# Optimization experiments

Hardware: AMD Instinct MI355X
Metric: run time of the kernel (lower is better)

## Reference

```python
import jax, jax.numpy as jnp
import numpy as np

B, C, H, W = 32, 256, 64, 64
AS = 8  # attn_size


def _avgpool(x, s):
    # exact adaptive avg pool when H,W divisible by s: mean over each block
    b, c, h, w = x.shape
    return x.reshape(b, c, s, h // s, s, w // s).mean(axis=(3, 5))


def setup_inputs() -> dict:
    key = jax.random.key(0)
    ks = jax.random.split(key, 6)
    scale = 1.0 / np.sqrt(C)
    return {
        "F_rgb": jax.random.normal(ks[0], (B, C, H, W), jnp.float32),
        "F_d": jax.random.normal(ks[1], (B, C, H, W), jnp.float32),
        "Wq": jax.random.normal(ks[2], (C, C), jnp.float32) * scale,
        "bq": jnp.zeros((C,), jnp.float32),
        "Wk": jax.random.normal(ks[3], (C, C), jnp.float32) * scale,
        "bk": jnp.zeros((C,), jnp.float32),
        "Wv": jax.random.normal(ks[4], (C, C), jnp.float32) * scale,
        "bv": jnp.zeros((C,), jnp.float32),
        "alpha": jnp.float32(0.5),
    }


def reference(F_rgb, F_d, Wq, bq, Wk, bk, Wv, bv, alpha):
    b, c, h_in, w_in = F_rgb.shape
    R = _avgpool(F_rgb, AS)  # [B,C,8,8]
    D = _avgpool(F_d, AS)    # [B,C,8,8]
    # 1x1 convs == channel-mixing matmuls
    Q = jnp.einsum('oc,bchw->bohw', Wq, R) + bq[None, :, None, None]
    K = jnp.einsum('oc,bchw->bohw', Wk, D) + bk[None, :, None, None]
    V = jnp.einsum('oc,bchw->bohw', Wv, D) + bv[None, :, None, None]
    T = AS * AS
    Qf = Q.reshape(b, c, T)
    Kf = K.reshape(b, c, T)
    Vf = V.reshape(b, c, T)
    A = jnp.einsum('bct,bcs->bts', Qf, Kf)        # [B,T,T]
    A = jax.nn.softmax(A, axis=-1)
    Fatt = jnp.einsum('bcs,bts->bct', Vf, A)      # V @ A^T
    Fatt = Fatt.reshape(b, c, AS, AS)
    # bilinear upsample, half-pixel centers (== torch align_corners=False)
    Fatt = jax.image.resize(Fatt, (b, c, h_in, w_in), method='bilinear')
    return alpha * Fatt + (1.0 - alpha) * F_rgb
```

## Files before the change

### kernel.cpp

```cpp
#include <hip/hip_runtime.h>
#include <math.h>

#define B_  32
#define C_  256
#define T_  64
#define HW_ 4096

__global__ __launch_bounds__(256) void k_pool(const float* __restrict__ Frgb,
                                              const float* __restrict__ Fd,
                                              float* __restrict__ R,
                                              float* __restrict__ D) {
    __shared__ float P[2][1024];
    const int tid = threadIdx.x;
    const int plane = blockIdx.x;
    const float4* pr = (const float4*)Frgb + (size_t)plane * 1024;
    const float4* pd = (const float4*)Fd   + (size_t)plane * 1024;
    #pragma unroll
    for (int k = 0; k < 4; ++k) {
        float4 a = pr[k*256 + tid];
        P[0][k*256 + tid] = a.x + a.y + a.z + a.w;
        float4 b = pd[k*256 + tid];
        P[1][k*256 + tid] = b.x + b.y + b.z + b.w;
    }
    __syncthreads();
    if (tid < 128) {
        const int tensor = tid >> 6;
        const int cell = tid & 63;
        const int cy = cell >> 3, cx = cell & 7;
        const int base = (cy >> 1)*256 + (cy & 1)*128 + 2*cx;
        float s = 0.f;
        #pragma unroll
        for (int rg = 0; rg < 8; ++rg)
            s += P[tensor][base + rg*16] + P[tensor][base + rg*16 + 1];
        float* dst = tensor ? D : R;
        dst[(size_t)plane*64 + cell] = s * (1.f/64.f);
    }
}

__global__ __launch_bounds__(256) void k_qkv(const float* __restrict__ R, const float* __restrict__ D,
                                             const float* __restrict__ Wq, const float* __restrict__ bq,
                                             const float* __restrict__ Wk, const float* __restrict__ bk,
                                             const float* __restrict__ Wv, const float* __restrict__ bv,
                                             float* __restrict__ Q, float* __restrict__ K,
                                             float* __restrict__ V) {
    __shared__ float Ws[32 * 256];
    const int tid = threadIdx.x;
    const int tbase = blockIdx.x * 16;
    const int b = blockIdx.y;
    const int z = blockIdx.z;
    const float* W    = (z == 0) ? Wq : (z == 1) ? Wk : Wv;
    const float* bias = (z == 0) ? bq : (z == 1) ? bk : bv;
    const float* X    = (z == 0) ? R  : D;
    float* Out        = (z == 0) ? Q  : (z == 1) ? K  : V;

    const int o = tid;
    float acc[16];
    const float bz = bias[o];
    #pragma unroll
    for (int t = 0; t < 16; ++t) acc[t] = bz;

    const float* Xb = X + (size_t)b * C_ * T_;
    for (int cb = 0; cb < 256; cb += 32) {
        __syncthreads();
        #pragma unroll
        for (int k = 0; k < 8; ++k) {
            float4 w4 = *(const float4*)(W + (size_t)o * 256 + cb + k*4);
            Ws[(k*4 + 0)*256 + o] = w4.x;
            Ws[(k*4 + 1)*256 + o] = w4.y;
            Ws[(k*4 + 2)*256 + o] = w4.z;
            Ws[(k*4 + 3)*256 + o] = w4.w;
        }
        __syncthreads();
        for (int cl = 0; cl < 32; ++cl) {
            const float w = Ws[cl*256 + o];
            const float* xrow = Xb + (size_t)(cb + cl) * T_ + tbase;
            #pragma unroll
            for (int t = 0; t < 16; ++t) acc[t] += w * xrow[t];
        }
    }
    float* orow = Out + ((size_t)b * C_ + o) * T_ + tbase;
    #pragma unroll
    for (int t = 0; t < 16; ++t) orow[t] = acc[t];
}

__global__ __launch_bounds__(256) void k_attnA(const float* __restrict__ Q,
                                               const float* __restrict__ K,
                                               float* __restrict__ AT) {
    __shared__ float Ks[128 * 64];
    __shared__ float As[64 * 65];
    const int tid  = threadIdx.x;
    const int lane = tid & 63;
    const int wv   = __builtin_amdgcn_readfirstlane(tid >> 6);
    const int b = blockIdx.x;

    float acc[16];
    #pragma unroll
    for (int t = 0; t < 16; ++t) acc[t] = 0.f;

    const float* Qb = Q + (size_t)b * C_ * T_;
    const float* Kb = K + (size_t)b * C_ * T_;
    for (int half = 0; half < 2; ++half) {
        __syncthreads();
        const float4* src = (const float4*)(Kb + half * 128 * 64);
        float4* dst = (float4*)Ks;
        #pragma unroll
        for (int k = 0; k < 8; ++k) dst[k*256 + tid] = src[k*256 + tid];
        __syncthreads();
        for (int cl = 0; cl < 128; ++cl) {
            const float kv = Ks[cl*64 + lane];
            const float* qrow = Qb + (size_t)(half*128 + cl) * T_ + wv*16;
            #pragma unroll
            for (int t = 0; t < 16; ++t) acc[t] += kv * qrow[t];
        }
    }

    #pragma unroll
    for (int t = 0; t < 16; ++t) {
        float m = acc[t];
        #pragma unroll
        for (int off = 32; off; off >>= 1) m = fmaxf(m, __shfl_xor(m, off));
        const float e = __expf(acc[t] - m);
        float ssum = e;
        #pragma unroll
        for (int off = 32; off; off >>= 1) ssum += __shfl_xor(ssum, off);
        As[lane*65 + wv*16 + t] = e / ssum;
    }
    __syncthreads();

    float* ATb = AT + (size_t)b * T_ * T_;
    #pragma unroll
    for (int i = 0; i < 16; ++i) {
        const int idx = i*256 + tid;
        const int s = idx >> 6, t = idx & 63;
        ATb[idx] = As[s*65 + t];
    }
}

__global__ __launch_bounds__(256) void k_up(const float* __restrict__ AT,
                                            const float* __restrict__ V,
                                            const float* __restrict__ Frgb,
                                            const float* __restrict__ alphap,
                                            float* __restrict__ Out) {
    __shared__ float Vs[64];
    __shared__ float Ps[4][64];
    __shared__ float Fs[64];
    const int tid = threadIdx.x;
    const int plane = blockIdx.x;
    const int b = plane >> 8;
    if (tid < 64) Vs[tid] = V[(size_t)plane*64 + tid];
    __syncthreads();
    {
        const int t = tid & 63;
        const int sq = tid >> 6;
        const float* ATb = AT + (size_t)b * T_ * T_;
        float sum = 0.f;
        #pragma unroll
        for (int j = 0; j < 16; ++j) {
            const int s = sq*16 + j;
            sum = fmaf(Vs[s], ATb[s*64 + t], sum);
        }
        Ps[sq][t] = sum;
    }
    __syncthreads();
    if (tid < 64) Fs[tid] = Ps[0][tid] + Ps[1][tid] + Ps[2][tid] + Ps[3][tid];
    __syncthreads();

    const float alpha = alphap[0];
    const float beta = 1.f - alpha;
    const float4* rgb4 = (const float4*)Frgb + (size_t)plane * 1024;
    float4* out4 = (float4*)Out + (size_t)plane * 1024;
    #pragma unroll
    for (int k = 0; k < 4; ++k) {
        const int flat = k*1024 + tid*4;
        const int y  = flat >> 6;
        const int xb = flat & 63;
        const float sy = y * 0.125f - 0.4375f;
        const float fy = floorf(sy);
        const float wy = sy - fy;
        const int iy = (int)fy;
        const int y0 = iy < 0 ? 0 : iy;
        const int y1 = (iy + 1) > 7 ? 7 : (iy + 1);
        float4 rv = rgb4[k*256 + tid];
        float o[4];
        const float rs[4] = {rv.x, rv.y, rv.z, rv.w};
        #pragma unroll
        for (int j = 0; j < 4; ++j) {
            const int x = xb + j;
            const float sx = x * 0.125f - 0.4375f;
            const float fx = floorf(sx);
            const float wx = sx - fx;
            const int ix = (int)fx;
            const int x0 = ix < 0 ? 0 : ix;
            const int x1 = (ix + 1) > 7 ? 7 : (ix + 1);
            const float top = (1.f - wx) * Fs[y0*8 + x0] + wx * Fs[y0*8 + x1];
            const float bot = (1.f - wx) * Fs[y1*8 + x0] + wx * Fs[y1*8 + x1];
            const float v = (1.f - wy) * top + wy * bot;
            o[j] = alpha * v + beta * rs[j];
        }
        out4[k*256 + tid] = make_float4(o[0], o[1], o[2], o[3]);
    }
}

extern "C" void kernel_launch(void* const* d_in, const int* in_sizes, int n_in,
                              void* d_out, int out_size, void* d_ws, size_t ws_size,
                              hipStream_t stream) {
    const float* Frgb  = (const float*)d_in[0];
    const float* Fd    = (const float*)d_in[1];
    const float* Wq    = (const float*)d_in[2];
    const float* bq    = (const float*)d_in[3];
    const float* Wk    = (const float*)d_in[4];
    const float* bk    = (const float*)d_in[5];
    const float* Wv    = (const float*)d_in[6];
    const float* bv    = (const float*)d_in[7];
    const float* alpha = (const float*)d_in[8];

    float* ws = (float*)d_ws;
    const size_t PC = (size_t)B_ * C_ * T_;
    float* R    = ws;
    float* D    = ws + PC;
    float* Q    = ws + 2*PC;
    float* K    = ws + 3*PC;
    float* V    = ws + 4*PC;
    float* AT   = ws + 5*PC;
    float* Out  = (float*)d_out;

    k_pool <<<B_*C_, 256, 0, stream>>>(Frgb, Fd, R, D);
    k_qkv  <<<dim3(4, 32, 3), 256, 0, stream>>>(R, D, Wq, bq, Wk, bk, Wv, bv, Q, K, V);
    k_attnA<<<B_, 256, 0, stream>>>(Q, K, AT);
    k_up   <<<B_*C_, 256, 0, stream>>>(AT, V, Frgb, alpha, Out);
}
```

Measured before the change: 419.0 us.

## Rework pooling into wave-per-plane shuffles and fuse V·Aᵀ into attention kernel

Pooling now gives each wavefront one plane, loading it into registers and reducing with cross-lane shuffles, with no shared-memory staging or block barrier. The QKV kernel gets a padded, coalesced weight transpose into shared memory and writes its output as float4. The V·Aᵀ product moves from the upsample kernel into the attention kernel, which writes Fatt in place over Q. The upsample kernel then only loads 64 values per plane and issues its Frgb loads early. The attention kernel now has only 32 blocks doing extra serial work, which could lengthen its runtime. Aliasing Fatt onto Q is safe only if every block reads just its own batch slice of Q, and it does.

```diff
diff --git a/kernel.cpp b/kernel.cpp
--- a/kernel.cpp
+++ b/kernel.cpp
@@ -6,35 +6,34 @@
 #define T_  64
 #define HW_ 4096
 
+__device__ __forceinline__ float pool_plane(const float4* __restrict__ p, int lane) {
+    float4 v[16];
+    #pragma unroll
+    for (int q = 0; q < 16; ++q) v[q] = p[q*64 + lane];
+    float res = 0.f;
+    #pragma unroll
+    for (int m = 0; m < 8; ++m) {
+        float s = (v[2*m].x + v[2*m].y + v[2*m].z + v[2*m].w)
+                + (v[2*m+1].x + v[2*m+1].y + v[2*m+1].z + v[2*m+1].w);
+        s += __shfl_xor(s, 1);
+        s += __shfl_xor(s, 16);
+        s += __shfl_xor(s, 32);
+        float g = __shfl(s, 2*(lane & 7));
+        res = ((lane >> 3) == m) ? g : res;
+    }
+    return res * (1.f/64.f);
+}
+
 __global__ __launch_bounds__(256) void k_pool(const float* __restrict__ Frgb,
                                               const float* __restrict__ Fd,
                                               float* __restrict__ R,
                                               float* __restrict__ D) {
-    __shared__ float P[2][1024];
-    const int tid = threadIdx.x;
-    const int plane = blockIdx.x;
-    const float4* pr = (const float4*)Frgb + (size_t)plane * 1024;
-    const float4* pd = (const float4*)Fd   + (size_t)plane * 1024;
-    #pragma unroll
-    for (int k = 0; k < 4; ++k) {
-        float4 a = pr[k*256 + tid];
-        P[0][k*256 + tid] = a.x + a.y + a.z + a.w;
-        float4 b = pd[k*256 + tid];
-        P[1][k*256 + tid] = b.x + b.y + b.z + b.w;
-    }
-    __syncthreads();
-    if (tid < 128) {
-        const int tensor = tid >> 6;
-        const int cell = tid & 63;
-        const int cy = cell >> 3, cx = cell & 7;
-        const int base = (cy >> 1)*256 + (cy & 1)*128 + 2*cx;
-        float s = 0.f;
-        #pragma unroll
-        for (int rg = 0; rg < 8; ++rg)
-            s += P[tensor][base + rg*16] + P[tensor][base + rg*16 + 1];
-        float* dst = tensor ? D : R;
-        dst[(size_t)plane*64 + cell] = s * (1.f/64.f);
-    }
+    const int lane  = threadIdx.x & 63;
+    const int plane = (blockIdx.x << 2) + (threadIdx.x >> 6);
+    const float4* pa = (const float4*)Frgb + (size_t)plane * 1024;
+    const float4* pb = (const float4*)Fd   + (size_t)plane * 1024;
+    R[(size_t)plane*64 + lane] = pool_plane(pa, lane);
+    D[(size_t)plane*64 + lane] = pool_plane(pb, lane);
 }
 
 __global__ __launch_bounds__(256) void k_qkv(const float* __restrict__ R, const float* __restrict__ D,
@@ -43,7 +42,7 @@
                                              const float* __restrict__ Wv, const float* __restrict__ bv,
                                              float* __restrict__ Q, float* __restrict__ K,
                                              float* __restrict__ V) {
-    __shared__ float Ws[32 * 256];
+    __shared__ float Ws[32 * 257];
     const int tid = threadIdx.x;
     const int tbase = blockIdx.x * 16;
     const int b = blockIdx.y;
@@ -60,32 +59,37 @@
     for (int t = 0; t < 16; ++t) acc[t] = bz;
 
     const float* Xb = X + (size_t)b * C_ * T_;
+    const int orow = tid >> 3;
+    const int c4   = (tid & 7) * 4;
     for (int cb = 0; cb < 256; cb += 32) {
         __syncthreads();
         #pragma unroll
-        for (int k = 0; k < 8; ++k) {
-            float4 w4 = *(const float4*)(W + (size_t)o * 256 + cb + k*4);
-            Ws[(k*4 + 0)*256 + o] = w4.x;
-            Ws[(k*4 + 1)*256 + o] = w4.y;
-            Ws[(k*4 + 2)*256 + o] = w4.z;
-            Ws[(k*4 + 3)*256 + o] = w4.w;
+        for (int p = 0; p < 8; ++p) {
+            const int orr = orow + p*32;
+            float4 w4 = *(const float4*)(W + (size_t)orr * 256 + cb + c4);
+            Ws[(c4 + 0)*257 + orr] = w4.x;
+            Ws[(c4 + 1)*257 + orr] = w4.y;
+            Ws[(c4 + 2)*257 + orr] = w4.z;
+            Ws[(c4 + 3)*257 + orr] = w4.w;
         }
         __syncthreads();
         for (int cl = 0; cl < 32; ++cl) {
-            const float w = Ws[cl*256 + o];
+            const float w = Ws[cl*257 + o];
             const float* xrow = Xb + (size_t)(cb + cl) * T_ + tbase;
             #pragma unroll
-            for (int t = 0; t < 16; ++t) acc[t] += w * xrow[t];
-        }
-    }
-    float* orow = Out + ((size_t)b * C_ + o) * T_ + tbase;
-    #pragma unroll
-    for (int t = 0; t < 16; ++t) orow[t] = acc[t];
-}
-
-__global__ __launch_bounds__(256) void k_attnA(const float* __restrict__ Q,
+            for (int t = 0; t < 16; ++t) acc[t] = fmaf(w, xrow[t], acc[t]);
+        }
+    }
+    float* orowp = Out + ((size_t)b * C_ + o) * T_ + tbase;
+    #pragma unroll
+    for (int t4 = 0; t4 < 4; ++t4)
+        *(float4*)(orowp + t4*4) = make_float4(acc[t4*4+0], acc[t4*4+1], acc[t4*4+2], acc[t4*4+3]);
+}
+
+__global__ __launch_bounds__(256) void k_attnA(const float* Q,
                                                const float* __restrict__ K,
-                                               float* __restrict__ AT) {
+                                               const float* __restrict__ V,
+                                               float* Fatt) {
     __shared__ float Ks[128 * 64];
     __shared__ float As[64 * 65];
     const int tid  = threadIdx.x;
@@ -110,7 +114,7 @@
             const float kv = Ks[cl*64 + lane];
             const float* qrow = Qb + (size_t)(half*128 + cl) * T_ + wv*16;
             #pragma unroll
-            for (int t = 0; t < 16; ++t) acc[t] += kv * qrow[t];
+            for (int t = 0; t < 16; ++t) acc[t] = fmaf(kv, qrow[t], acc[t]);
         }
     }
 
@@ -127,47 +131,37 @@
     }
     __syncthreads();
 
-    float* ATb = AT + (size_t)b * T_ * T_;
-    #pragma unroll
-    for (int i = 0; i < 16; ++i) {
-        const int idx = i*256 + tid;
-        const int s = idx >> 6, t = idx & 63;
-        ATb[idx] = As[s*65 + t];
-    }
-}
-
-__global__ __launch_bounds__(256) void k_up(const float* __restrict__ AT,
-                                            const float* __restrict__ V,
+    float at[64];
+    #pragma unroll
+    for (int s = 0; s < 64; ++s) at[s] = As[s*65 + lane];
+    const float* Vb = V + (size_t)b * C_ * T_;
+    float* Fb = Fatt + (size_t)b * C_ * T_;
+    for (int j = 0; j < 64; ++j) {
+        const int c = wv*64 + j;
+        const float* vr = Vb + (size_t)c * T_;
+        float sum = 0.f;
+        #pragma unroll
+        for (int s = 0; s < 64; ++s) sum = fmaf(vr[s], at[s], sum);
+        Fb[(size_t)c * T_ + lane] = sum;
+    }
+}
+
+__global__ __launch_bounds__(256) void k_up(const float* __restrict__ Fatt,
                                             const float* __restrict__ Frgb,
                                             const float* __restrict__ alphap,
                                             float* __restrict__ Out) {
-    __shared__ float Vs[64];
-    __shared__ float Ps[4][64];
     __shared__ float Fs[64];
     const int tid = threadIdx.x;
     const int plane = blockIdx.x;
-    const int b = plane >> 8;
-    if (tid < 64) Vs[tid] = V[(size_t)plane*64 + tid];
-    __syncthreads();
-    {
-        const int t = tid & 63;
-        const int sq = tid >> 6;
-        const float* ATb = AT + (size_t)b * T_ * T_;
-        float sum = 0.f;
-        #pragma unroll
-        for (int j = 0; j < 16; ++j) {
-            const int s = sq*16 + j;
-            sum = fmaf(Vs[s], ATb[s*64 + t], sum);
-        }
-        Ps[sq][t] = sum;
-    }
-    __syncthreads();
-    if (tid < 64) Fs[tid] = Ps[0][tid] + Ps[1][tid] + Ps[2][tid] + Ps[3][tid];
+    const float4* rgb4 = (const float4*)Frgb + (size_t)plane * 1024;
+    float4 rv[4];
+    #pragma unroll
+    for (int k = 0; k < 4; ++k) rv[k] = rgb4[k*256 + tid];
+    if (tid < 64) Fs[tid] = Fatt[(size_t)plane*64 + tid];
     __syncthreads();
 
     const float alpha = alphap[0];
     const float beta = 1.f - alpha;
-    const float4* rgb4 = (const float4*)Frgb + (size_t)plane * 1024;
     float4* out4 = (float4*)Out + (size_t)plane * 1024;
     #pragma unroll
     for (int k = 0; k < 4; ++k) {
@@ -180,9 +174,8 @@
         const int iy = (int)fy;
         const int y0 = iy < 0 ? 0 : iy;
         const int y1 = (iy + 1) > 7 ? 7 : (iy + 1);
-        float4 rv = rgb4[k*256 + tid];
+        const float rs[4] = {rv[k].x, rv[k].y, rv[k].z, rv[k].w};
         float o[4];
-        const float rs[4] = {rv.x, rv.y, rv.z, rv.w};
         #pragma unroll
         for (int j = 0; j < 4; ++j) {
             const int x = xb + j;
@@ -221,11 +214,11 @@
     float* Q    = ws + 2*PC;
     float* K    = ws + 3*PC;
     float* V    = ws + 4*PC;
-    float* AT   = ws + 5*PC;
+    float* Fatt = Q;
     float* Out  = (float*)d_out;
 
-    k_pool <<<B_*C_, 256, 0, stream>>>(Frgb, Fd, R, D);
+    k_pool <<<2048, 256, 0, stream>>>(Frgb, Fd, R, D);
     k_qkv  <<<dim3(4, 32, 3), 256, 0, stream>>>(R, D, Wq, bq, Wk, bk, Wv, bv, Q, K, V);
-    k_attnA<<<B_, 256, 0, stream>>>(Q, K, AT);
-    k_up   <<<B_*C_, 256, 0, stream>>>(AT, V, Frgb, alpha, Out);
-}
+    k_attnA<<<B_, 256, 0, stream>>>(Q, K, V, Fatt);
+    k_up   <<<B_*C_, 256, 0, stream>>>(Fatt, Frgb, alpha, Out);
+}
```

Result: slower. 473.7 us (+13.0%).

## Split pooling per tensor, widen qkv/attn grids, coalesce weight loads, prefetch rgb

Applied to the files above, without the earlier changes.

The pooling kernel is split into one launch per input tensor, each block reducing a single plane. The QKV projection now runs twice as many blocks, each computing 8 time steps instead of 16. Its weight tile is loaded row-coalesced into a padded shared array, and results are written as float4. The attention-score kernel moves to 512 threads with 8 columns per wave. The upsample kernel issues its F_rgb loads before the small V·A reduction so memory latency overlaps with that compute. Together these aim to raise parallelism and memory efficiency, at the cost of an extra kernel launch and more blocks that each re-read X.

```diff
diff --git a/kernel.cpp b/kernel.cpp
--- a/kernel.cpp
+++ b/kernel.cpp
@@ -6,34 +6,26 @@
 #define T_  64
 #define HW_ 4096
 
-__global__ __launch_bounds__(256) void k_pool(const float* __restrict__ Frgb,
-                                              const float* __restrict__ Fd,
-                                              float* __restrict__ R,
-                                              float* __restrict__ D) {
-    __shared__ float P[2][1024];
+__global__ __launch_bounds__(256) void k_pool1(const float* __restrict__ In,
+                                               float* __restrict__ Outp) {
+    __shared__ float P[1024];
     const int tid = threadIdx.x;
     const int plane = blockIdx.x;
-    const float4* pr = (const float4*)Frgb + (size_t)plane * 1024;
-    const float4* pd = (const float4*)Fd   + (size_t)plane * 1024;
+    const float4* p = (const float4*)In + (size_t)plane * 1024;
     #pragma unroll
     for (int k = 0; k < 4; ++k) {
-        float4 a = pr[k*256 + tid];
-        P[0][k*256 + tid] = a.x + a.y + a.z + a.w;
-        float4 b = pd[k*256 + tid];
-        P[1][k*256 + tid] = b.x + b.y + b.z + b.w;
-    }
-    __syncthreads();
-    if (tid < 128) {
-        const int tensor = tid >> 6;
-        const int cell = tid & 63;
-        const int cy = cell >> 3, cx = cell & 7;
+        float4 a = p[k*256 + tid];
+        P[k*256 + tid] = a.x + a.y + a.z + a.w;
+    }
+    __syncthreads();
+    if (tid < 64) {
+        const int cy = tid >> 3, cx = tid & 7;
         const int base = (cy >> 1)*256 + (cy & 1)*128 + 2*cx;
         float s = 0.f;
         #pragma unroll
         for (int rg = 0; rg < 8; ++rg)
-            s += P[tensor][base + rg*16] + P[tensor][base + rg*16 + 1];
-        float* dst = tensor ? D : R;
-        dst[(size_t)plane*64 + cell] = s * (1.f/64.f);
+            s += P[base + rg*16] + P[base + rg*16 + 1];
+        Outp[(size_t)plane*64 + tid] = s * (1.f/64.f);
     }
 }
 
@@ -43,9 +35,9 @@
                                              const float* __restrict__ Wv, const float* __restrict__ bv,
                                              float* __restrict__ Q, float* __restrict__ K,
                                              float* __restrict__ V) {
-    __shared__ float Ws[32 * 256];
+    __shared__ float Ws[32 * 257];
     const int tid = threadIdx.x;
-    const int tbase = blockIdx.x * 16;
+    const int tbase = blockIdx.x * 8;
     const int b = blockIdx.y;
     const int z = blockIdx.z;
     const float* W    = (z == 0) ? Wq : (z == 1) ? Wk : Wv;
@@ -54,36 +46,39 @@
     float* Out        = (z == 0) ? Q  : (z == 1) ? K  : V;
 
     const int o = tid;
-    float acc[16];
+    float acc[8];
     const float bz = bias[o];
     #pragma unroll
-    for (int t = 0; t < 16; ++t) acc[t] = bz;
+    for (int t = 0; t < 8; ++t) acc[t] = bz;
 
     const float* Xb = X + (size_t)b * C_ * T_;
+    const int orow = tid >> 3;
+    const int c4   = (tid & 7) * 4;
     for (int cb = 0; cb < 256; cb += 32) {
         __syncthreads();
         #pragma unroll
-        for (int k = 0; k < 8; ++k) {
-            float4 w4 = *(const float4*)(W + (size_t)o * 256 + cb + k*4);
-            Ws[(k*4 + 0)*256 + o] = w4.x;
-            Ws[(k*4 + 1)*256 + o] = w4.y;
-            Ws[(k*4 + 2)*256 + o] = w4.z;
-            Ws[(k*4 + 3)*256 + o] = w4.w;
+        for (int p = 0; p < 8; ++p) {
+            const int orr = orow + p*32;
+            float4 w4 = *(const float4*)(W + (size_t)orr * 256 + cb + c4);
+            Ws[(c4 + 0)*257 + orr] = w4.x;
+            Ws[(c4 + 1)*257 + orr] = w4.y;
+            Ws[(c4 + 2)*257 + orr] = w4.z;
+            Ws[(c4 + 3)*257 + orr] = w4.w;
         }
         __syncthreads();
         for (int cl = 0; cl < 32; ++cl) {
-            const float w = Ws[cl*256 + o];
+            const float w = Ws[cl*257 + o];
             const float* xrow = Xb + (size_t)(cb + cl) * T_ + tbase;
             #pragma unroll
-            for (int t = 0; t < 16; ++t) acc[t] += w * xrow[t];
-        }
-    }
-    float* orow = Out + ((size_t)b * C_ + o) * T_ + tbase;
-    #pragma unroll
-    for (int t = 0; t < 16; ++t) orow[t] = acc[t];
-}
-
-__global__ __launch_bounds__(256) void k_attnA(const float* __restrict__ Q,
+            for (int t = 0; t < 8; ++t) acc[t] = fmaf(w, xrow[t], acc[t]);
+        }
+    }
+    float* orowp = Out + ((size_t)b * C_ + o) * T_ + tbase;
+    *(float4*)(orowp + 0) = make_float4(acc[0], acc[1], acc[2], acc[3]);
+    *(float4*)(orowp + 4) = make_float4(acc[4], acc[5], acc[6], acc[7]);
+}
+
+__global__ __launch_bounds__(512) void k_attnA(const float* __restrict__ Q,
                                                const float* __restrict__ K,
                                                float* __restrict__ AT) {
     __shared__ float Ks[128 * 64];
@@ -93,9 +88,9 @@
     const int wv   = __builtin_amdgcn_readfirstlane(tid >> 6);
     const int b = blockIdx.x;
 
-    float acc[16];
-    #pragma unroll
-    for (int t = 0; t < 16; ++t) acc[t] = 0.f;
+    float acc[8];
+    #pragma unroll
+    for (int t = 0; t < 8; ++t) acc[t] = 0.f;
 
     const float* Qb = Q + (size_t)b * C_ * T_;
     const float* Kb = K + (size_t)b * C_ * T_;
@@ -104,18 +99,18 @@
         const float4* src = (const float4*)(Kb + half * 128 * 64);
         float4* dst = (float4*)Ks;
         #pragma unroll
-        for (int k = 0; k < 8; ++k) dst[k*256 + tid] = src[k*256 + tid];
+        for (int k = 0; k < 4; ++k) dst[k*512 + tid] = src[k*512 + tid];
         __syncthreads();
         for (int cl = 0; cl < 128; ++cl) {
             const float kv = Ks[cl*64 + lane];
-            const float* qrow = Qb + (size_t)(half*128 + cl) * T_ + wv*16;
+            const float* qrow = Qb + (size_t)(half*128 + cl) * T_ + wv*8;
             #pragma unroll
-            for (int t = 0; t < 16; ++t) acc[t] += kv * qrow[t];
-        }
-    }
-
-    #pragma unroll
-    for (int t = 0; t < 16; ++t) {
+            for (int t = 0; t < 8; ++t) acc[t] = fmaf(kv, qrow[t], acc[t]);
+        }
+    }
+
+    #pragma unroll
+    for (int t = 0; t < 8; ++t) {
         float m = acc[t];
         #pragma unroll
         for (int off = 32; off; off >>= 1) m = fmaxf(m, __shfl_xor(m, off));
@@ -123,14 +118,14 @@
         float ssum = e;
         #pragma unroll
         for (int off = 32; off; off >>= 1) ssum += __shfl_xor(ssum, off);
-        As[lane*65 + wv*16 + t] = e / ssum;
+        As[lane*65 + wv*8 + t] = e / ssum;
     }
     __syncthreads();
 
     float* ATb = AT + (size_t)b * T_ * T_;
     #pragma unroll
-    for (int i = 0; i < 16; ++i) {
-        const int idx = i*256 + tid;
+    for (int i = 0; i < 8; ++i) {
+        const int idx = i*512 + tid;
         const int s = idx >> 6, t = idx & 63;
         ATb[idx] = As[s*65 + t];
     }
@@ -147,6 +142,12 @@
     const int tid = threadIdx.x;
     const int plane = blockIdx.x;
     const int b = plane >> 8;
+
+    const float4* rgb4 = (const float4*)Frgb + (size_t)plane * 1024;
+    float4 rv[4];
+    #pragma unroll
+    for (int k = 0; k < 4; ++k) rv[k] = rgb4[k*256 + tid];
+
     if (tid < 64) Vs[tid] = V[(size_t)plane*64 + tid];
     __syncthreads();
     {
@@ -167,7 +168,6 @@
 
     const float alpha = alphap[0];
     const float beta = 1.f - alpha;
-    const float4* rgb4 = (const float4*)Frgb + (size_t)plane * 1024;
     float4* out4 = (float4*)Out + (size_t)plane * 1024;
     #pragma unroll
     for (int k = 0; k < 4; ++k) {
@@ -180,9 +180,8 @@
         const int iy = (int)fy;
         const int y0 = iy < 0 ? 0 : iy;
         const int y1 = (iy + 1) > 7 ? 7 : (iy + 1);
-        float4 rv = rgb4[k*256 + tid];
+        const float rs[4] = {rv[k].x, rv[k].y, rv[k].z, rv[k].w};
         float o[4];
-        const float rs[4] = {rv.x, rv.y, rv.z, rv.w};
         #pragma unroll
         for (int j = 0; j < 4; ++j) {
             const int x = xb + j;
@@ -224,8 +223,9 @@
     float* AT   = ws + 5*PC;
     float* Out  = (float*)d_out;
 
-    k_pool <<<B_*C_, 256, 0, stream>>>(Frgb, Fd, R, D);
-    k_qkv  <<<dim3(4, 32, 3), 256, 0, stream>>>(R, D, Wq, bq, Wk, bk, Wv, bv, Q, K, V);
-    k_attnA<<<B_, 256, 0, stream>>>(Q, K, AT);
+    k_pool1<<<B_*C_, 256, 0, stream>>>(Frgb, R);
+    k_pool1<<<B_*C_, 256, 0, stream>>>(Fd,   D);
+    k_qkv  <<<dim3(8, 32, 3), 256, 0, stream>>>(R, D, Wq, bq, Wk, bk, Wv, bv, Q, K, V);
+    k_attnA<<<B_, 512, 0, stream>>>(Q, K, AT);
     k_up   <<<B_*C_, 256, 0, stream>>>(AT, V, Frgb, alpha, Out);
 }
```

Result: faster. 397.9 us (-5.0%).
